# Kernel tuning notes

Measured on AMD Instinct MI355X. Metric: run time of the kernel, lower is better.

Reference implementation:

```python
import jax, jax.numpy as jnp
import numpy as np

TEMPERATURE = 8.0  # sqrt(k_dim=64)
NEG = -2.0 ** 15   # masked_fill value from the torch module


def setup_inputs() -> dict:
    key = jax.random.key(0)
    kq, kk, kv, km = jax.random.split(key, 4)
    B, H, N, L, D = 4, 8, 128, 128, 64
    q = jax.random.normal(kq, (B, H, N, L, D), dtype=jnp.float32)
    k = jax.random.normal(kk, (B, H, N, L, D), dtype=jnp.float32)
    v = jax.random.normal(kv, (B, H, N, L, D), dtype=jnp.float32)
    mask = jax.random.randint(km, (B, 1, N, L, L), 0, 2, dtype=jnp.int32)
    return {"q": q, "k": k, "v": v, "mask": mask}


def reference(q, k, v, mask):
    # attn: [B,H,N,Lq,Lk] = q [B,H,N,Lq,D] @ k^T [B,H,N,D,Lk]
    attn = jnp.einsum('bhnqd,bhnkd->bhnqk', q, k) / TEMPERATURE
    attn = jnp.where(mask == 0, jnp.float32(NEG), attn)
    attn = jax.nn.softmax(attn, axis=-1)
    # dropout is identity in eval mode
    out = jnp.einsum('bhnqk,bhnkd->bhnqd', attn, v)
    return out
```

## Files before the change

### kernel.cpp

```cpp
#include <hip/hip_runtime.h>
#include <hip/hip_bf16.h>


typedef __bf16 bf16;
typedef bf16 bf16x4 __attribute__((ext_vector_type(4)));
typedef bf16 bf16x8 __attribute__((ext_vector_type(8)));
typedef float f32x4 __attribute__((ext_vector_type(4)));

#define MFMA16(a, b, c) __builtin_amdgcn_mfma_f32_16x16x32_bf16((a), (b), (c), 0, 0, 0)

__global__ __launch_bounds__(256, 2) void attn_head_kernel(
    const float* __restrict__ q, const float* __restrict__ k,
    const float* __restrict__ v, const int* __restrict__ mask,
    float* __restrict__ out)
{
    constexpr int H = 8, N = 128, L = 128, D = 64;

    __shared__ bf16 KL[128][72];
    __shared__ bf16 VT[64][136];
    __shared__ bf16 PL[4][32][40];

    int bid = blockIdx.x;
    int l   = (bid & 7) * 512 + (bid >> 3);
    int h   = l & 7;
    int n   = (l >> 3) & 127;
    int b   = l >> 10;

    const size_t base = (((size_t)(b * H + h)) * N + n) * (size_t)(L * D);
    const float* Qp = q + base;
    const float* Kp = k + base;
    const float* Vp = v + base;
    float*       Op = out + base;
    const int*   Mp = mask + ((size_t)(b * N + n)) * (size_t)(L * L);

    const int tid  = threadIdx.x;
    const int wave = tid >> 6;
    const int lane = tid & 63;
    const int g    = lane >> 4;
    const int c    = lane & 15;

    #pragma unroll
    for (int i = 0; i < 8; ++i) {
        int e   = i * 256 + tid;
        int row = e >> 4;
        int d0  = (e & 15) * 4;
        float4 kv = ((const float4*)Kp)[e];
        bf16x4 pk = { (bf16)kv.x, (bf16)kv.y, (bf16)kv.z, (bf16)kv.w };
        *(bf16x4*)&KL[row][d0] = pk;
        float4 vv = ((const float4*)Vp)[e];
        VT[d0 + 0][row] = (bf16)vv.x;
        VT[d0 + 1][row] = (bf16)vv.y;
        VT[d0 + 2][row] = (bf16)vv.z;
        VT[d0 + 3][row] = (bf16)vv.w;
    }

    bf16x8 qa[2][2];
    #pragma unroll
    for (int rt = 0; rt < 2; ++rt)
        #pragma unroll
        for (int ds = 0; ds < 2; ++ds) {
            int row = wave * 32 + rt * 16 + c;
            int d0  = ds * 32 + g * 8;
            const float4* p = (const float4*)(Qp + row * D + d0);
            float4 x0 = p[0], x1 = p[1];
            bf16x8 f = { (bf16)x0.x, (bf16)x0.y, (bf16)x0.z, (bf16)x0.w,
                         (bf16)x1.x, (bf16)x1.y, (bf16)x1.z, (bf16)x1.w };
            qa[rt][ds] = f;
        }

    __syncthreads();

    f32x4 acc[2][8];
    #pragma unroll
    for (int rt = 0; rt < 2; ++rt)
        #pragma unroll
        for (int ct = 0; ct < 8; ++ct)
            acc[rt][ct] = (f32x4){0.f, 0.f, 0.f, 0.f};

    #pragma unroll
    for (int ct = 0; ct < 8; ++ct) {
        bf16x8 kb0 = *(const bf16x8*)&KL[ct * 16 + c][g * 8];
        bf16x8 kb1 = *(const bf16x8*)&KL[ct * 16 + c][32 + g * 8];
        #pragma unroll
        for (int rt = 0; rt < 2; ++rt) {
            acc[rt][ct] = MFMA16(qa[rt][0], kb0, acc[rt][ct]);
            acc[rt][ct] = MFMA16(qa[rt][1], kb1, acc[rt][ct]);
        }
    }

    float rinv[2][4];
    #pragma unroll
    for (int rt = 0; rt < 2; ++rt)
        #pragma unroll
        for (int j = 0; j < 4; ++j) {
            int row = wave * 32 + rt * 16 + g * 4 + j;
            const int* mrow = Mp + row * L;
            float vv[8];
            float mx = -3.4e38f;
            #pragma unroll
            for (int ct = 0; ct < 8; ++ct) {
                float s = acc[rt][ct][j] * 0.125f;
                int m = mrow[ct * 16 + c];
                s = (m == 0) ? -32768.0f : s;
                vv[ct] = s;
                mx = fmaxf(mx, s);
            }
            mx = fmaxf(mx, __shfl_xor(mx, 1));
            mx = fmaxf(mx, __shfl_xor(mx, 2));
            mx = fmaxf(mx, __shfl_xor(mx, 4));
            mx = fmaxf(mx, __shfl_xor(mx, 8));
            float sum = 0.f;
            #pragma unroll
            for (int ct = 0; ct < 8; ++ct) {
                float e = __expf(vv[ct] - mx);
                acc[rt][ct][j] = e;
                sum += e;
            }
            sum += __shfl_xor(sum, 1);
            sum += __shfl_xor(sum, 2);
            sum += __shfl_xor(sum, 4);
            sum += __shfl_xor(sum, 8);
            rinv[rt][j] = __builtin_amdgcn_rcpf(sum);
        }

    f32x4 oacc[2][4];
    #pragma unroll
    for (int rt = 0; rt < 2; ++rt)
        #pragma unroll
        for (int dt = 0; dt < 4; ++dt)
            oacc[rt][dt] = (f32x4){0.f, 0.f, 0.f, 0.f};

    for (int kc = 0; kc < 4; ++kc) {
        #pragma unroll
        for (int rt = 0; rt < 2; ++rt)
            #pragma unroll
            for (int cc = 0; cc < 2; ++cc) {
                int ct = kc * 2 + cc;
                #pragma unroll
                for (int j = 0; j < 4; ++j)
                    PL[wave][rt * 16 + g * 4 + j][cc * 16 + c] = (bf16)acc[rt][ct][j];
            }
        __syncthreads();

        bf16x8 vb[4];
        #pragma unroll
        for (int dt = 0; dt < 4; ++dt)
            vb[dt] = *(const bf16x8*)&VT[dt * 16 + c][kc * 32 + g * 8];
        #pragma unroll
        for (int rt = 0; rt < 2; ++rt) {
            bf16x8 pa = *(const bf16x8*)&PL[wave][rt * 16 + c][g * 8];
            #pragma unroll
            for (int dt = 0; dt < 4; ++dt)
                oacc[rt][dt] = MFMA16(pa, vb[dt], oacc[rt][dt]);
        }
        __syncthreads();
    }

    #pragma unroll
    for (int rt = 0; rt < 2; ++rt)
        #pragma unroll
        for (int j = 0; j < 4; ++j) {
            int row = wave * 32 + rt * 16 + g * 4 + j;
            float invs = rinv[rt][j];
            float* orow = Op + row * D;
            #pragma unroll
            for (int dt = 0; dt < 4; ++dt)
                orow[dt * 16 + c] = oacc[rt][dt][j] * invs;
        }
}

extern "C" void kernel_launch(void* const* d_in, const int* in_sizes, int n_in,
                              void* d_out, int out_size, void* d_ws, size_t ws_size,
                              hipStream_t stream) {
    const float* q    = (const float*)d_in[0];
    const float* k    = (const float*)d_in[1];
    const float* v    = (const float*)d_in[2];
    const int*   mask = (const int*)d_in[3];
    float*       out  = (float*)d_out;
    attn_head_kernel<<<4096, 256, 0, stream>>>(q, k, v, mask, out);
}
```

Before: 131.2 us.

## Transpose QK^T MFMA, reuse K LDS for P, vectorize mask and V loads

Computes S^T by swapping the MFMA operands, so each lane holds one query row. Mask loads become int4 and the softmax reductions need only two shuffles. The probability staging buffer now aliases the K region of LDS, cutting shared memory so launch bounds can be raised to four blocks per CU. The V transpose uses vectorized bf16x4 LDS writes, 1/8 is folded into Q before the bf16 cast, and normalization moves before the PV matmul, which removes the per-chunk block barriers. The trade-offs are extra register pressure under the tighter launch bound and a slight change in rounding from scaling before bf16 conversion.

After: 118.2 us. 9.9% less time.

```diff
diff --git a/kernel.cpp b/kernel.cpp
--- a/kernel.cpp
+++ b/kernel.cpp
@@ -9,22 +9,20 @@
 
 #define MFMA16(a, b, c) __builtin_amdgcn_mfma_f32_16x16x32_bf16((a), (b), (c), 0, 0, 0)
 
-__global__ __launch_bounds__(256, 2) void attn_head_kernel(
+__global__ __launch_bounds__(256, 4) void attn_head_kernel(
     const float* __restrict__ q, const float* __restrict__ k,
     const float* __restrict__ v, const int* __restrict__ mask,
     float* __restrict__ out)
 {
     constexpr int H = 8, N = 128, L = 128, D = 64;
 
-    __shared__ bf16 KL[128][72];
-    __shared__ bf16 VT[64][136];
-    __shared__ bf16 PL[4][32][40];
-
-    int bid = blockIdx.x;
-    int l   = (bid & 7) * 512 + (bid >> 3);
-    int h   = l & 7;
-    int n   = (l >> 3) & 127;
-    int b   = l >> 10;
+    __shared__ __align__(16) char SMEM[35840];
+    bf16 (*KL)[72]  = (bf16(*)[72])SMEM;
+    bf16 (*VT)[136] = (bf16(*)[136])(SMEM + 18432);
+
+    int bid  = blockIdx.x;
+    int lidx = (bid & 7) * 512 + (bid >> 3);
+    int h = lidx & 7, n = (lidx >> 3) & 127, b = lidx >> 10;
 
     const size_t base = (((size_t)(b * H + h)) * N + n) * (size_t)(L * D);
     const float* Qp = q + base;
@@ -47,125 +45,149 @@
         float4 kv = ((const float4*)Kp)[e];
         bf16x4 pk = { (bf16)kv.x, (bf16)kv.y, (bf16)kv.z, (bf16)kv.w };
         *(bf16x4*)&KL[row][d0] = pk;
-        float4 vv = ((const float4*)Vp)[e];
-        VT[d0 + 0][row] = (bf16)vv.x;
-        VT[d0 + 1][row] = (bf16)vv.y;
-        VT[d0 + 2][row] = (bf16)vv.z;
-        VT[d0 + 3][row] = (bf16)vv.w;
-    }
-
-    bf16x8 qa[2][2];
+    }
+    #pragma unroll
+    for (int i = 0; i < 2; ++i) {
+        int id = i * 256 + tid;
+        int db = id & 15;
+        int kb = id >> 4;
+        const float4* vp = (const float4*)(Vp + kb * 4 * 64 + db * 4);
+        float4 r0 = vp[0], r1 = vp[16], r2 = vp[32], r3 = vp[48];
+        bf16x4 w0 = { (bf16)r0.x, (bf16)r1.x, (bf16)r2.x, (bf16)r3.x };
+        bf16x4 w1 = { (bf16)r0.y, (bf16)r1.y, (bf16)r2.y, (bf16)r3.y };
+        bf16x4 w2 = { (bf16)r0.z, (bf16)r1.z, (bf16)r2.z, (bf16)r3.z };
+        bf16x4 w3 = { (bf16)r0.w, (bf16)r1.w, (bf16)r2.w, (bf16)r3.w };
+        *(bf16x4*)&VT[db * 4 + 0][kb * 4] = w0;
+        *(bf16x4*)&VT[db * 4 + 1][kb * 4] = w1;
+        *(bf16x4*)&VT[db * 4 + 2][kb * 4] = w2;
+        *(bf16x4*)&VT[db * 4 + 3][kb * 4] = w3;
+    }
+
+    bf16x8 qb[2][2];
     #pragma unroll
     for (int rt = 0; rt < 2; ++rt)
         #pragma unroll
         for (int ds = 0; ds < 2; ++ds) {
             int row = wave * 32 + rt * 16 + c;
-            int d0  = ds * 32 + g * 8;
-            const float4* p = (const float4*)(Qp + row * D + d0);
+            const float4* p = (const float4*)(Qp + row * D + ds * 32 + g * 8);
             float4 x0 = p[0], x1 = p[1];
-            bf16x8 f = { (bf16)x0.x, (bf16)x0.y, (bf16)x0.z, (bf16)x0.w,
-                         (bf16)x1.x, (bf16)x1.y, (bf16)x1.z, (bf16)x1.w };
-            qa[rt][ds] = f;
+            bf16x8 f = { (bf16)(x0.x * 0.125f), (bf16)(x0.y * 0.125f),
+                         (bf16)(x0.z * 0.125f), (bf16)(x0.w * 0.125f),
+                         (bf16)(x1.x * 0.125f), (bf16)(x1.y * 0.125f),
+                         (bf16)(x1.z * 0.125f), (bf16)(x1.w * 0.125f) };
+            qb[rt][ds] = f;
         }
 
     __syncthreads();
 
-    f32x4 acc[2][8];
+    f32x4 acc[8][2];
+    #pragma unroll
+    for (int kt = 0; kt < 8; ++kt)
+        #pragma unroll
+        for (int rt = 0; rt < 2; ++rt)
+            acc[kt][rt] = (f32x4){0.f, 0.f, 0.f, 0.f};
+
+    #pragma unroll
+    for (int kt = 0; kt < 8; ++kt) {
+        bf16x8 ka0 = *(const bf16x8*)&KL[kt * 16 + c][g * 8];
+        bf16x8 ka1 = *(const bf16x8*)&KL[kt * 16 + c][32 + g * 8];
+        #pragma unroll
+        for (int rt = 0; rt < 2; ++rt) {
+            acc[kt][rt] = MFMA16(ka0, qb[rt][0], acc[kt][rt]);
+            acc[kt][rt] = MFMA16(ka1, qb[rt][1], acc[kt][rt]);
+        }
+    }
+
+    __syncthreads();
+
+    float rinv[2];
+    #pragma unroll
+    for (int rt = 0; rt < 2; ++rt) {
+        int qrow = wave * 32 + rt * 16 + c;
+        const int* mrow = Mp + (size_t)qrow * L;
+        int4 mm[8];
+        #pragma unroll
+        for (int kt = 0; kt < 8; ++kt)
+            mm[kt] = *(const int4*)(mrow + kt * 16 + g * 4);
+        float mx = -3.0e38f;
+        #pragma unroll
+        for (int kt = 0; kt < 8; ++kt) {
+            float s0 = mm[kt].x ? acc[kt][rt][0] : -32768.f;
+            float s1 = mm[kt].y ? acc[kt][rt][1] : -32768.f;
+            float s2 = mm[kt].z ? acc[kt][rt][2] : -32768.f;
+            float s3 = mm[kt].w ? acc[kt][rt][3] : -32768.f;
+            acc[kt][rt][0] = s0; acc[kt][rt][1] = s1;
+            acc[kt][rt][2] = s2; acc[kt][rt][3] = s3;
+            mx = fmaxf(mx, fmaxf(fmaxf(s0, s1), fmaxf(s2, s3)));
+        }
+        mx = fmaxf(mx, __shfl_xor(mx, 16));
+        mx = fmaxf(mx, __shfl_xor(mx, 32));
+        float sum = 0.f;
+        #pragma unroll
+        for (int kt = 0; kt < 8; ++kt) {
+            #pragma unroll
+            for (int j = 0; j < 4; ++j) {
+                float e = __expf(acc[kt][rt][j] - mx);
+                acc[kt][rt][j] = e;
+                sum += e;
+            }
+        }
+        sum += __shfl_xor(sum, 16);
+        sum += __shfl_xor(sum, 32);
+        rinv[rt] = __builtin_amdgcn_rcpf(sum);
+    }
+
+    bf16* PLw = (bf16*)(SMEM + wave * 4608);
+    f32x4 oacc[2][4];
     #pragma unroll
     for (int rt = 0; rt < 2; ++rt)
         #pragma unroll
-        for (int ct = 0; ct < 8; ++ct)
-            acc[rt][ct] = (f32x4){0.f, 0.f, 0.f, 0.f};
-
-    #pragma unroll
-    for (int ct = 0; ct < 8; ++ct) {
-        bf16x8 kb0 = *(const bf16x8*)&KL[ct * 16 + c][g * 8];
-        bf16x8 kb1 = *(const bf16x8*)&KL[ct * 16 + c][32 + g * 8];
+        for (int dt = 0; dt < 4; ++dt)
+            oacc[rt][dt] = (f32x4){0.f, 0.f, 0.f, 0.f};
+
+    #pragma unroll
+    for (int p = 0; p < 2; ++p) {
         #pragma unroll
         for (int rt = 0; rt < 2; ++rt) {
-            acc[rt][ct] = MFMA16(qa[rt][0], kb0, acc[rt][ct]);
-            acc[rt][ct] = MFMA16(qa[rt][1], kb1, acc[rt][ct]);
-        }
-    }
-
-    float rinv[2][4];
+            float r = rinv[rt];
+            #pragma unroll
+            for (int t = 0; t < 4; ++t) {
+                f32x4 a = acc[p * 4 + t][rt];
+                bf16x4 w = { (bf16)(a[0] * r), (bf16)(a[1] * r),
+                             (bf16)(a[2] * r), (bf16)(a[3] * r) };
+                *(bf16x4*)&PLw[(rt * 16 + c) * 72 + t * 16 + g * 4] = w;
+            }
+        }
+        asm volatile("s_waitcnt lgkmcnt(0)" ::: "memory");
+        __builtin_amdgcn_sched_barrier(0);
+
+        #pragma unroll
+        for (int kc2 = 0; kc2 < 2; ++kc2) {
+            int kc = p * 2 + kc2;
+            bf16x8 vb[4];
+            #pragma unroll
+            for (int dt = 0; dt < 4; ++dt)
+                vb[dt] = *(const bf16x8*)&VT[dt * 16 + c][kc * 32 + g * 8];
+            #pragma unroll
+            for (int rt = 0; rt < 2; ++rt) {
+                bf16x8 pa = *(const bf16x8*)&PLw[(rt * 16 + c) * 72 + kc2 * 32 + g * 8];
+                #pragma unroll
+                for (int dt = 0; dt < 4; ++dt)
+                    oacc[rt][dt] = MFMA16(pa, vb[dt], oacc[rt][dt]);
+            }
+        }
+        asm volatile("" ::: "memory");
+    }
+
     #pragma unroll
     for (int rt = 0; rt < 2; ++rt)
         #pragma unroll
         for (int j = 0; j < 4; ++j) {
             int row = wave * 32 + rt * 16 + g * 4 + j;
-            const int* mrow = Mp + row * L;
-            float vv[8];
-            float mx = -3.4e38f;
-            #pragma unroll
-            for (int ct = 0; ct < 8; ++ct) {
-                float s = acc[rt][ct][j] * 0.125f;
-                int m = mrow[ct * 16 + c];
-                s = (m == 0) ? -32768.0f : s;
-                vv[ct] = s;
-                mx = fmaxf(mx, s);
-            }
-            mx = fmaxf(mx, __shfl_xor(mx, 1));
-            mx = fmaxf(mx, __shfl_xor(mx, 2));
-            mx = fmaxf(mx, __shfl_xor(mx, 4));
-            mx = fmaxf(mx, __shfl_xor(mx, 8));
-            float sum = 0.f;
-            #pragma unroll
-            for (int ct = 0; ct < 8; ++ct) {
-                float e = __expf(vv[ct] - mx);
-                acc[rt][ct][j] = e;
-                sum += e;
-            }
-            sum += __shfl_xor(sum, 1);
-            sum += __shfl_xor(sum, 2);
-            sum += __shfl_xor(sum, 4);
-            sum += __shfl_xor(sum, 8);
-            rinv[rt][j] = __builtin_amdgcn_rcpf(sum);
-        }
-
-    f32x4 oacc[2][4];
-    #pragma unroll
-    for (int rt = 0; rt < 2; ++rt)
-        #pragma unroll
-        for (int dt = 0; dt < 4; ++dt)
-            oacc[rt][dt] = (f32x4){0.f, 0.f, 0.f, 0.f};
-
-    for (int kc = 0; kc < 4; ++kc) {
-        #pragma unroll
-        for (int rt = 0; rt < 2; ++rt)
-            #pragma unroll
-            for (int cc = 0; cc < 2; ++cc) {
-                int ct = kc * 2 + cc;
-                #pragma unroll
-                for (int j = 0; j < 4; ++j)
-                    PL[wave][rt * 16 + g * 4 + j][cc * 16 + c] = (bf16)acc[rt][ct][j];
-            }
-        __syncthreads();
-
-        bf16x8 vb[4];
-        #pragma unroll
-        for (int dt = 0; dt < 4; ++dt)
-            vb[dt] = *(const bf16x8*)&VT[dt * 16 + c][kc * 32 + g * 8];
-        #pragma unroll
-        for (int rt = 0; rt < 2; ++rt) {
-            bf16x8 pa = *(const bf16x8*)&PL[wave][rt * 16 + c][g * 8];
+            float* orow = Op + row * D;
             #pragma unroll
             for (int dt = 0; dt < 4; ++dt)
-                oacc[rt][dt] = MFMA16(pa, vb[dt], oacc[rt][dt]);
-        }
-        __syncthreads();
-    }
-
-    #pragma unroll
-    for (int rt = 0; rt < 2; ++rt)
-        #pragma unroll
-        for (int j = 0; j < 4; ++j) {
-            int row = wave * 32 + rt * 16 + g * 4 + j;
-            float invs = rinv[rt][j];
-            float* orow = Op + row * D;
-            #pragma unroll
-            for (int dt = 0; dt < 4; ++dt)
-                orow[dt * 16 + c] = oacc[rt][dt][j] * invs;
+                orow[dt * 16 + c] = oacc[rt][dt][j];
         }
 }
 
```
